# Kernel optimization log

Measured on AMD Instinct MI355X. Metric: run time of the kernel, lower is better.

## Reference

```python
import jax, jax.numpy as jnp
import numpy as np

B, N, DIM = 2, 2048, 1024
NUM_HEADS = 16
EFF = NUM_HEADS // 2          # 8 effective heads
HD = DIM // NUM_HEADS         # 64
LAMBDA_INIT = 0.8
EPS = 1e-5


def setup_inputs() -> dict:
    key = jax.random.key(0)
    ks = jax.random.split(key, 16)
    s = 0.02
    return {
        "x":  jax.random.normal(ks[0], (B, N, DIM), dtype=jnp.float32),
        "Wq": jax.random.normal(ks[1], (DIM, DIM), dtype=jnp.float32) * s,
        "bq": jnp.zeros((DIM,), dtype=jnp.float32),
        "Wk": jax.random.normal(ks[2], (DIM, DIM), dtype=jnp.float32) * s,
        "bk": jnp.zeros((DIM,), dtype=jnp.float32),
        "Wv": jax.random.normal(ks[3], (DIM, DIM), dtype=jnp.float32) * s,
        "bv": jnp.zeros((DIM,), dtype=jnp.float32),
        "Wo": jax.random.normal(ks[4], (DIM, DIM), dtype=jnp.float32) * s,
        "bo": jnp.zeros((DIM,), dtype=jnp.float32),
        "norm_w": jnp.ones((2 * HD,), dtype=jnp.float32),
        "lq1": jax.random.normal(ks[5], (HD,), dtype=jnp.float32) * 0.1,
        "lk1": jax.random.normal(ks[6], (HD,), dtype=jnp.float32) * 0.1,
        "lq2": jax.random.normal(ks[7], (HD,), dtype=jnp.float32) * 0.1,
        "lk2": jax.random.normal(ks[8], (HD,), dtype=jnp.float32) * 0.1,
    }


def reference(x, Wq, bq, Wk, bk, Wv, bv, Wo, bo, norm_w, lq1, lk1, lq2, lk2):
    scale = HD ** -0.5
    # projections (torch Linear: y = x @ W.T + b)
    q = (x @ Wq.T + bq).reshape(B, N, NUM_HEADS, HD).transpose(0, 2, 1, 3) * scale  # [B,2E,N,hd]
    k = (x @ Wk.T + bk).reshape(B, N, NUM_HEADS, HD).transpose(0, 2, 1, 3)          # [B,2E,N,hd]
    v = (x @ Wv.T + bv).reshape(B, N, EFF, 2 * HD).transpose(0, 2, 1, 3)            # [B,E,N,2hd]

    scores = jnp.einsum('bhqd,bhkd->bhqk', q, k)              # [B,2E,N,N]
    probs = jax.nn.softmax(scores, axis=-1)
    probs = probs.reshape(B, EFF, 2, N, N)                    # pair consecutive heads

    lam = jnp.exp(jnp.sum(lq1 * lk1)) - jnp.exp(jnp.sum(lq2 * lk2)) + LAMBDA_INIT
    diff = probs[:, :, 0] - lam * probs[:, :, 1]              # [B,E,N,N]

    out = jnp.einsum('behk,bekd->behd'.replace('e','h').replace('hh','h') if False else 'bhqk,bhkd->bhqd', diff, v)  # [B,E,N,2hd]
    # headwise RMSNorm over last dim (2*hd)
    out = out * jax.lax.rsqrt(jnp.mean(out * out, axis=-1, keepdims=True) + EPS) * norm_w
    out = out * (1.0 - LAMBDA_INIT)

    out = out.transpose(0, 2, 1, 3).reshape(B, N, DIM)
    return out @ Wo.T + bo
```

## Files before the change

### kernel.cpp

```cpp
#include <hip/hip_runtime.h>
#include <hip/hip_bf16.h>

#define B_   2
#define N_   2048
#define DIM_ 1024
#define HD_  64
#define DV_  128

typedef __bf16 bf16;
typedef __bf16 bf16x8 __attribute__((ext_vector_type(8)));
typedef __bf16 bf16x4 __attribute__((ext_vector_type(4)));
typedef float  floatx4 __attribute__((ext_vector_type(4)));
typedef float  floatx16 __attribute__((ext_vector_type(16)));
typedef unsigned int uint;
typedef uint uint2v __attribute__((ext_vector_type(2)));
typedef uint uint4v __attribute__((ext_vector_type(4)));

#if __has_builtin(__builtin_amdgcn_exp2f)
#define EXP2(x) __builtin_amdgcn_exp2f(x)
#else
#define EXP2(x) exp2f(x)
#endif

#define QSCALE 0.1803368801111244f

__device__ __forceinline__ void async16(const void* g, void* l) {
  __builtin_amdgcn_global_load_lds(
      (__attribute__((address_space(1))) void*)g,
      (__attribute__((address_space(3))) void*)l, 16, 0, 0);
}

__device__ __forceinline__ uint packbf(float a, float b) {
  unsigned short ul = __builtin_bit_cast(unsigned short, (bf16)a);
  unsigned short uh = __builtin_bit_cast(unsigned short, (bf16)b);
  return (uint)ul | ((uint)uh << 16);
}

__global__ void convert_kernel(const float* __restrict__ x,
                               const float* __restrict__ wq,
                               const float* __restrict__ wk,
                               const float* __restrict__ wv,
                               const float* __restrict__ wo,
                               bf16* __restrict__ dst) {
  const int NX = B_ * N_ * DIM_;
  const int NW = DIM_ * DIM_;
  int i = (blockIdx.x * 256 + threadIdx.x) * 4;
  const float* src;
  int off;
  if (i < NX) { src = x; off = i; }
  else {
    int j = i - NX;
    int w = j >> 20;
    off = j & (NW - 1);
    src = (w == 0) ? wq : (w == 1) ? wk : (w == 2) ? wv : wo;
  }
  float4 v = *(const float4*)(src + off);
  bf16x4 o = { (bf16)v.x, (bf16)v.y, (bf16)v.z, (bf16)v.w };
  *(bf16x4*)(dst + i) = o;
}

__global__ __launch_bounds__(256) void proj_kernel(
    const bf16* __restrict__ xb, const bf16* __restrict__ wall,
    const float* __restrict__ bq, const float* __restrict__ bk,
    const float* __restrict__ bv,
    bf16* __restrict__ qo, bf16* __restrict__ ko, bf16* __restrict__ vt) {
  __shared__ __align__(16) bf16 SM[2 * 128 * 64];
  bf16* At = SM;
  bf16* Bt = SM + 128 * 64;
  const int tid = threadIdx.x, lane = tid & 63, w = tid >> 6;
  const int tm = blockIdx.x, tn = blockIdx.y, z = blockIdx.z;
  const int quad = lane >> 4, l15 = lane & 15;
  const int wm = (w >> 1) * 64, wn = (w & 1) * 64;
  const bf16* Ab = xb + (long)tm * 128 * DIM_;
  const bf16* Bb = wall + (long)z * (DIM_ * DIM_) + (long)tn * 128 * DIM_;
  floatx4 zero = {0.f, 0.f, 0.f, 0.f};
  floatx4 acc[4][4];
#pragma unroll
  for (int i = 0; i < 4; ++i)
#pragma unroll
    for (int j = 0; j < 4; ++j) acc[i][j] = zero;

  for (int kb = 0; kb < DIM_ / 64; ++kb) {
    for (int idx = tid; idx < 1024; idx += 256) {
      int row = idx >> 3, ch = idx & 7, g = ch ^ (row & 7);
      async16(Ab + row * DIM_ + kb * 64 + g * 8, (char*)At + (idx - lane) * 16);
      async16(Bb + row * DIM_ + kb * 64 + g * 8, (char*)Bt + (idx - lane) * 16);
    }
    __syncthreads();
#pragma unroll
    for (int ks = 0; ks < 2; ++ks) {
      bf16x8 af[4], bfm[4];
#pragma unroll
      for (int mt = 0; mt < 4; ++mt) {
        int r = wm + mt * 16 + l15;
        af[mt] = *(const bf16x8*)&At[r * 64 + ((ks * 4 + quad) ^ (r & 7)) * 8];
      }
#pragma unroll
      for (int nt = 0; nt < 4; ++nt) {
        int r = wn + nt * 16 + l15;
        bfm[nt] = *(const bf16x8*)&Bt[r * 64 + ((ks * 4 + quad) ^ (r & 7)) * 8];
      }
#pragma unroll
      for (int mt = 0; mt < 4; ++mt)
#pragma unroll
        for (int nt = 0; nt < 4; ++nt)
          acc[mt][nt] = __builtin_amdgcn_mfma_f32_16x16x32_bf16(
              af[mt], bfm[nt], acc[mt][nt], 0, 0, 0);
    }
    __syncthreads();
  }

  if (z != 2) {
#pragma unroll
    for (int mt = 0; mt < 4; ++mt)
#pragma unroll
      for (int nt = 0; nt < 4; ++nt)
#pragma unroll
        for (int r = 0; r < 4; ++r) {
          int grow = tm * 128 + wm + mt * 16 + quad * 4 + r;
          int gcol = tn * 128 + wn + nt * 16 + l15;
          float v = acc[mt][nt][r];
          if (z == 0) {
            qo[(long)grow * DIM_ + gcol] = (bf16)((v + bq[gcol]) * QSCALE);
          } else {
            ko[(long)grow * DIM_ + gcol] = (bf16)(v + bk[gcol]);
          }
        }
  } else {
    bf16* Vl = SM;
#pragma unroll
    for (int nt = 0; nt < 4; ++nt) {
      int d = wn + nt * 16 + l15;
      float bvv = bv[tn * 128 + d];
      int m = (d & 7) * 2;
#pragma unroll
      for (int mt = 0; mt < 4; ++mt) {
        bf16x4 v4 = { (bf16)(acc[mt][nt][0] + bvv), (bf16)(acc[mt][nt][1] + bvv),
                      (bf16)(acc[mt][nt][2] + bvv), (bf16)(acc[mt][nt][3] + bvv) };
        int c = (wm >> 2) + mt * 4 + quad;
        *(bf16x4*)&Vl[d * 128 + (c ^ m) * 4] = v4;
      }
    }
    __syncthreads();
    const int bb = tm >> 4, e = tn;
    const long rowbase = ((long)(bb * 8 + e) * 128) * (long)N_ + (tm & 15) * 128;
#pragma unroll
    for (int p = 0; p < 8; ++p) {
      int d = p * 16 + (tid >> 4), j = tid & 15;
      int cs = (2 * j) ^ ((d & 7) * 2);
      bf16x8 val = *(const bf16x8*)&Vl[d * 128 + cs * 4];
      *(bf16x8*)&vt[rowbase + (long)d * N_ + j * 8] = val;
    }
  }
}

__global__ __launch_bounds__(256, 2) void attn_kernel(
    const bf16* __restrict__ qb, const bf16* __restrict__ kbuf,
    const bf16* __restrict__ vt,
    const float* __restrict__ lq1, const float* __restrict__ lk1,
    const float* __restrict__ lq2, const float* __restrict__ lk2,
    const float* __restrict__ norm_w, bf16* __restrict__ ao) {
  __shared__ __align__(16) char smem[65536];

  const int tid = threadIdx.x, lane = tid & 63, w = tid >> 6;
  const int qt = blockIdx.x, e = blockIdx.y, b = blockIdx.z;
  const int hl = w & 1, qh = w >> 1;
  const int h = lane >> 5, l31 = lane & 31;
  const int qbase = qt * 64;

  bf16x8 qf[4];
  {
    const bf16* qrp = qb + (long)(b * N_ + qbase + qh * 32 + l31) * DIM_
                      + e * 128 + hl * 64 + h * 8;
#pragma unroll
    for (int c = 0; c < 4; ++c) qf[c] = *(const bf16x8*)(qrp + c * 16);
  }

  const bf16* kbase = kbuf + (long)b * N_ * DIM_ + e * 128;
  const bf16* vbase = vt + (long)(b * 8 + e) * DV_ * N_;

  floatx16 acc[4];
#pragma unroll
  for (int dt = 0; dt < 4; ++dt) acc[dt] = floatx16{};
  float lp = 0.f;

#define STAGE(ktv, bufv)                                                            \
  {                                                                                 \
    int kt_ = (ktv);                                                                \
    char* kdst = smem + (bufv) * 16384;                                             \
    char* vdst = smem + 32768 + (bufv) * 16384;                                     \
    _Pragma("unroll") for (int t = 0; t < 4; ++t) {                                 \
      int idx = tid + t * 256;                                                      \
      int khl = idx >> 9, row = (idx >> 3) & 63, ch = idx & 7;                      \
      int g = ch ^ (row & 7) ^ ((row >> 3) & 3);                                    \
      async16(kbase + ((long)(kt_ * 64 + row)) * DIM_ + khl * 64 + g * 8,           \
              kdst + (idx - lane) * 16);                                            \
    }                                                                               \
    _Pragma("unroll") for (int t = 0; t < 4; ++t) {                                 \
      int idx = tid + t * 256;                                                      \
      int row = idx >> 3, ch = idx & 7;                                             \
      int g = ch ^ (row & 7) ^ ((row >> 3) & 3);                                    \
      async16(vbase + (long)row * N_ + kt_ * 64 + g * 8,                            \
              vdst + (idx - lane) * 16);                                            \
    }                                                                               \
  }

  STAGE(0, 0);

  for (int kt = 0; kt < N_ / 64; ++kt) {
    const int buf = kt & 1;
    __syncthreads();
    if (kt + 1 < N_ / 64) STAGE(kt + 1, buf ^ 1);

    const bf16* Kh = (const bf16*)(smem + buf * 16384) + hl * 4096;
    const bf16* Vb = (const bf16*)(smem + 32768 + buf * 16384);

    bf16x8 kfrag[2][4], vfrag[4][4];
#pragma unroll
    for (int kt2 = 0; kt2 < 2; ++kt2)
#pragma unroll
      for (int c = 0; c < 4; ++c) {
        int row = kt2 * 32 + l31;
        int sw = (c * 2 + h) ^ (row & 7) ^ ((row >> 3) & 3);
        kfrag[kt2][c] = *(const bf16x8*)&Kh[row * 64 + sw * 8];
      }
#pragma unroll
    for (int dt = 0; dt < 4; ++dt)
#pragma unroll
      for (int kc = 0; kc < 4; ++kc) {
        int row = dt * 32 + l31;
        int sw = (kc * 2 + h) ^ (row & 7) ^ ((row >> 3) & 3);
        vfrag[dt][kc] = *(const bf16x8*)&Vb[row * 64 + sw * 8];
      }

    bf16x8 af[2][2];
#pragma unroll
    for (int kt2 = 0; kt2 < 2; ++kt2) {
      floatx16 sv{};
      __builtin_amdgcn_s_setprio(1);
#pragma unroll
      for (int c = 0; c < 4; ++c)
        sv = __builtin_amdgcn_mfma_f32_32x32x16_bf16(kfrag[kt2][c], qf[c], sv, 0, 0, 0);
      __builtin_amdgcn_s_setprio(0);
      float t[16];
      float s = 0.f;
#pragma unroll
      for (int i = 0; i < 16; ++i) { t[i] = EXP2(sv[i]); s += t[i]; }
      lp += s;
      uint d0 = packbf(t[0], t[1]),   d1 = packbf(t[2], t[3]);
      uint d2 = packbf(t[4], t[5]),   d3 = packbf(t[6], t[7]);
      uint d4 = packbf(t[8], t[9]),   d5 = packbf(t[10], t[11]);
      uint d6 = packbf(t[12], t[13]), d7 = packbf(t[14], t[15]);
      uint4v f0, f1;
#if __has_builtin(__builtin_amdgcn_permlane32_swap)
      uint2v r02 = __builtin_amdgcn_permlane32_swap(d0, d2, false, false);
      uint2v r13 = __builtin_amdgcn_permlane32_swap(d1, d3, false, false);
      f0 = uint4v{r02.x, r13.x, r02.y, r13.y};
      uint2v r46 = __builtin_amdgcn_permlane32_swap(d4, d6, false, false);
      uint2v r57 = __builtin_amdgcn_permlane32_swap(d5, d7, false, false);
      f1 = uint4v{r46.x, r57.x, r46.y, r57.y};
#else
      uint e0 = __shfl_xor((int)d0, 32, 64), e1 = __shfl_xor((int)d1, 32, 64);
      uint e2 = __shfl_xor((int)d2, 32, 64), e3 = __shfl_xor((int)d3, 32, 64);
      uint e4 = __shfl_xor((int)d4, 32, 64), e5 = __shfl_xor((int)d5, 32, 64);
      uint e6 = __shfl_xor((int)d6, 32, 64), e7 = __shfl_xor((int)d7, 32, 64);
      f0 = h ? uint4v{e2, e3, d2, d3} : uint4v{d0, d1, e0, e1};
      f1 = h ? uint4v{e6, e7, d6, d7} : uint4v{d4, d5, e4, e5};
#endif
      af[kt2][0] = __builtin_bit_cast(bf16x8, f0);
      af[kt2][1] = __builtin_bit_cast(bf16x8, f1);
    }
    __builtin_amdgcn_s_setprio(1);
#pragma unroll
    for (int dt = 0; dt < 4; ++dt)
#pragma unroll
      for (int kt2 = 0; kt2 < 2; ++kt2)
#pragma unroll
        for (int u = 0; u < 2; ++u)
          acc[dt] = __builtin_amdgcn_mfma_f32_32x32x16_bf16(
              af[kt2][u], vfrag[dt][kt2 * 2 + u], acc[dt], 0, 0, 0);
    __builtin_amdgcn_s_setprio(0);
  }

  lp += __shfl_xor(lp, 32, 64);

  float* Ob = (float*)smem;
  __syncthreads();

  if (hl == 1) {
#pragma unroll
    for (int r = 0; r < 16; ++r) {
      int qloc = (r & 3) + 8 * (r >> 2) + 4 * h;
      float inv = 1.0f / __shfl(lp, qloc, 64);
      float* row = &Ob[(qh * 32 + qloc) * 128 + l31];
#pragma unroll
      for (int dt = 0; dt < 4; ++dt) row[dt * 32] = acc[dt][r] * inv;
    }
  }
  __syncthreads();
  if (hl == 0) {
    float la = lq1[lane] * lk1[lane];
    float lb = lq2[lane] * lk2[lane];
#pragma unroll
    for (int m = 1; m < 64; m <<= 1) {
      la += __shfl_xor(la, m, 64);
      lb += __shfl_xor(lb, m, 64);
    }
    float lam = __expf(la) - __expf(lb) + 0.8f;
    float nw4[4];
#pragma unroll
    for (int dt = 0; dt < 4; ++dt) nw4[dt] = norm_w[dt * 32 + l31] * 0.2f;
#pragma unroll
    for (int r = 0; r < 16; ++r) {
      int qloc = (r & 3) + 8 * (r >> 2) + 4 * h;
      float inv = 1.0f / __shfl(lp, qloc, 64);
      const float* row = &Ob[(qh * 32 + qloc) * 128 + l31];
      float v[4], ss = 0.f;
#pragma unroll
      for (int dt = 0; dt < 4; ++dt) {
        v[dt] = acc[dt][r] * inv - lam * row[dt * 32];
        ss += v[dt] * v[dt];
      }
#pragma unroll
      for (int msk = 1; msk < 32; msk <<= 1) ss += __shfl_xor(ss, msk, 64);
      float rms = rsqrtf(ss * (1.0f / 128.0f) + 1e-5f);
      int n = qbase + qh * 32 + qloc;
      bf16* dst = ao + (long)(b * N_ + n) * DIM_ + e * DV_ + l31;
#pragma unroll
      for (int dt = 0; dt < 4; ++dt) dst[dt * 32] = (bf16)(v[dt] * rms * nw4[dt]);
    }
  }
}

__global__ __launch_bounds__(512) void out_gemm(
    const bf16* __restrict__ ab, const bf16* __restrict__ wo,
    const float* __restrict__ bo, float* __restrict__ out) {
  __shared__ __align__(16) bf16 At[128 * 64];
  __shared__ __align__(16) bf16 Bt[128 * 64];
  const int tid = threadIdx.x, lane = tid & 63, w = tid >> 6;
  const int tm = blockIdx.x, tn = blockIdx.y;
  const int quad = lane >> 4, l15 = lane & 15;
  const int wm = (w & 3) * 32, wn = (w >> 2) * 64;
  const bf16* Ab = ab + (long)tm * 128 * DIM_;
  const bf16* Bb = wo + (long)tn * 128 * DIM_;
  floatx4 zero = {0.f, 0.f, 0.f, 0.f};
  floatx4 acc[2][4];
#pragma unroll
  for (int i = 0; i < 2; ++i)
#pragma unroll
    for (int j = 0; j < 4; ++j) acc[i][j] = zero;

  for (int kb = 0; kb < DIM_ / 64; ++kb) {
    for (int idx = tid; idx < 1024; idx += 512) {
      int row = idx >> 3, ch = idx & 7, g = ch ^ (row & 7);
      async16(Ab + row * DIM_ + kb * 64 + g * 8, (char*)At + (idx - lane) * 16);
      async16(Bb + row * DIM_ + kb * 64 + g * 8, (char*)Bt + (idx - lane) * 16);
    }
    __syncthreads();
#pragma unroll
    for (int ks = 0; ks < 2; ++ks) {
      bf16x8 af[2], bfm[4];
#pragma unroll
      for (int mt = 0; mt < 2; ++mt) {
        int r = wm + mt * 16 + l15;
        af[mt] = *(const bf16x8*)&At[r * 64 + ((ks * 4 + quad) ^ (r & 7)) * 8];
      }
#pragma unroll
      for (int nt = 0; nt < 4; ++nt) {
        int r = wn + nt * 16 + l15;
        bfm[nt] = *(const bf16x8*)&Bt[r * 64 + ((ks * 4 + quad) ^ (r & 7)) * 8];
      }
#pragma unroll
      for (int mt = 0; mt < 2; ++mt)
#pragma unroll
        for (int nt = 0; nt < 4; ++nt)
          acc[mt][nt] = __builtin_amdgcn_mfma_f32_16x16x32_bf16(
              af[mt], bfm[nt], acc[mt][nt], 0, 0, 0);
    }
    __syncthreads();
  }
#pragma unroll
  for (int mt = 0; mt < 2; ++mt)
#pragma unroll
    for (int nt = 0; nt < 4; ++nt)
#pragma unroll
      for (int r = 0; r < 4; ++r) {
        int grow = tm * 128 + wm + mt * 16 + quad * 4 + r;
        int gcol = tn * 128 + wn + nt * 16 + l15;
        out[(long)grow * DIM_ + gcol] = acc[mt][nt][r] + bo[gcol];
      }
}

extern "C" void kernel_launch(void* const* d_in, const int* in_sizes, int n_in,
                              void* d_out, int out_size, void* d_ws, size_t ws_size,
                              hipStream_t stream) {
  const float* x    = (const float*)d_in[0];
  const float* Wq   = (const float*)d_in[1];
  const float* bq   = (const float*)d_in[2];
  const float* Wk   = (const float*)d_in[3];
  const float* bk   = (const float*)d_in[4];
  const float* Wv   = (const float*)d_in[5];
  const float* bv   = (const float*)d_in[6];
  const float* Wo   = (const float*)d_in[7];
  const float* bo   = (const float*)d_in[8];
  const float* nw   = (const float*)d_in[9];
  const float* lq1  = (const float*)d_in[10];
  const float* lk1  = (const float*)d_in[11];
  const float* lq2  = (const float*)d_in[12];
  const float* lk2  = (const float*)d_in[13];

  char* ws = (char*)d_ws;
  bf16* xb   = (bf16*)(ws + 256);
  bf16* wqb  = xb + 4194304;
  bf16* qb   = wqb + 4 * 1048576;
  bf16* kbuf = qb + 4194304;
  bf16* vtb  = kbuf + 4194304;
  bf16* ab   = vtb + 4194304;

  convert_kernel<<<8192, 256, 0, stream>>>(x, Wq, Wk, Wv, Wo, xb);
  proj_kernel<<<dim3(32, 8, 3), 256, 0, stream>>>(xb, wqb, bq, bk, bv, qb, kbuf, vtb);
  attn_kernel<<<dim3(32, 8, 2), 256, 0, stream>>>(qb, kbuf, vtb, lq1, lk1, lq2, lk2,
                                                  nw, ab);
  out_gemm<<<dim3(32, 8), 512, 0, stream>>>(ab, wqb + 3 * 1048576, bo, (float*)d_out);
}
```

Before: 219.9 us.

## Load attention K/V fragments directly from global memory with larger tiles

```diff
diff --git a/kernel.cpp b/kernel.cpp
--- a/kernel.cpp
+++ b/kernel.cpp
@@ -154,19 +154,20 @@
   }
 }
 
-__global__ __launch_bounds__(256, 2) void attn_kernel(
+__global__ __launch_bounds__(512, 2) void attn_kernel(
     const bf16* __restrict__ qb, const bf16* __restrict__ kbuf,
     const bf16* __restrict__ vt,
     const float* __restrict__ lq1, const float* __restrict__ lk1,
     const float* __restrict__ lq2, const float* __restrict__ lk2,
     const float* __restrict__ norm_w, bf16* __restrict__ ao) {
-  __shared__ __align__(16) char smem[65536];
+  __shared__ __align__(16) float Ob[128 * 128];
 
   const int tid = threadIdx.x, lane = tid & 63, w = tid >> 6;
-  const int qt = blockIdx.x, e = blockIdx.y, b = blockIdx.z;
+  const int swz = (blockIdx.x & 7) * 32 + (blockIdx.x >> 3);
+  const int qt = swz & 15, e = (swz >> 4) & 7, b = swz >> 7;
   const int hl = w & 1, qh = w >> 1;
   const int h = lane >> 5, l31 = lane & 31;
-  const int qbase = qt * 64;
+  const int qbase = qt * 128;
 
   bf16x8 qf[4];
   {
@@ -176,62 +177,29 @@
     for (int c = 0; c < 4; ++c) qf[c] = *(const bf16x8*)(qrp + c * 16);
   }
 
-  const bf16* kbase = kbuf + (long)b * N_ * DIM_ + e * 128;
-  const bf16* vbase = vt + (long)(b * 8 + e) * DV_ * N_;
+  const bf16* krow = kbuf + (long)b * N_ * DIM_ + (long)l31 * DIM_
+                     + e * 128 + hl * 64 + h * 8;
+  const bf16* vrow = vt + (long)(b * 8 + e) * DV_ * N_ + (long)l31 * N_ + h * 8;
 
   floatx16 acc[4];
 #pragma unroll
   for (int dt = 0; dt < 4; ++dt) acc[dt] = floatx16{};
   float lp = 0.f;
 
-#define STAGE(ktv, bufv)                                                            \
-  {                                                                                 \
-    int kt_ = (ktv);                                                                \
-    char* kdst = smem + (bufv) * 16384;                                             \
-    char* vdst = smem + 32768 + (bufv) * 16384;                                     \
-    _Pragma("unroll") for (int t = 0; t < 4; ++t) {                                 \
-      int idx = tid + t * 256;                                                      \
-      int khl = idx >> 9, row = (idx >> 3) & 63, ch = idx & 7;                      \
-      int g = ch ^ (row & 7) ^ ((row >> 3) & 3);                                    \
-      async16(kbase + ((long)(kt_ * 64 + row)) * DIM_ + khl * 64 + g * 8,           \
-              kdst + (idx - lane) * 16);                                            \
-    }                                                                               \
-    _Pragma("unroll") for (int t = 0; t < 4; ++t) {                                 \
-      int idx = tid + t * 256;                                                      \
-      int row = idx >> 3, ch = idx & 7;                                             \
-      int g = ch ^ (row & 7) ^ ((row >> 3) & 3);                                    \
-      async16(vbase + (long)row * N_ + kt_ * 64 + g * 8,                            \
-              vdst + (idx - lane) * 16);                                            \
-    }                                                                               \
-  }
-
-  STAGE(0, 0);
-
   for (int kt = 0; kt < N_ / 64; ++kt) {
-    const int buf = kt & 1;
-    __syncthreads();
-    if (kt + 1 < N_ / 64) STAGE(kt + 1, buf ^ 1);
-
-    const bf16* Kh = (const bf16*)(smem + buf * 16384) + hl * 4096;
-    const bf16* Vb = (const bf16*)(smem + 32768 + buf * 16384);
-
     bf16x8 kfrag[2][4], vfrag[4][4];
+    const bf16* kp = krow + (long)kt * 64 * DIM_;
 #pragma unroll
     for (int kt2 = 0; kt2 < 2; ++kt2)
 #pragma unroll
-      for (int c = 0; c < 4; ++c) {
-        int row = kt2 * 32 + l31;
-        int sw = (c * 2 + h) ^ (row & 7) ^ ((row >> 3) & 3);
-        kfrag[kt2][c] = *(const bf16x8*)&Kh[row * 64 + sw * 8];
-      }
+      for (int c = 0; c < 4; ++c)
+        kfrag[kt2][c] = *(const bf16x8*)(kp + (long)kt2 * 32 * DIM_ + c * 16);
+    const bf16* vp = vrow + kt * 64;
 #pragma unroll
     for (int dt = 0; dt < 4; ++dt)
 #pragma unroll
-      for (int kc = 0; kc < 4; ++kc) {
-        int row = dt * 32 + l31;
-        int sw = (kc * 2 + h) ^ (row & 7) ^ ((row >> 3) & 3);
-        vfrag[dt][kc] = *(const bf16x8*)&Vb[row * 64 + sw * 8];
-      }
+      for (int kc = 0; kc < 4; ++kc)
+        vfrag[dt][kc] = *(const bf16x8*)(vp + (long)dt * 32 * N_ + kc * 16);
 
     bf16x8 af[2][2];
 #pragma unroll
@@ -284,9 +252,6 @@
 
   lp += __shfl_xor(lp, 32, 64);
 
-  float* Ob = (float*)smem;
-  __syncthreads();
-
   if (hl == 1) {
 #pragma unroll
     for (int r = 0; r < 16; ++r) {
@@ -419,7 +384,6 @@
 
   convert_kernel<<<8192, 256, 0, stream>>>(x, Wq, Wk, Wv, Wo, xb);
   proj_kernel<<<dim3(32, 8, 3), 256, 0, stream>>>(xb, wqb, bq, bk, bv, qb, kbuf, vtb);
-  attn_kernel<<<dim3(32, 8, 2), 256, 0, stream>>>(qb, kbuf, vtb, lq1, lk1, lq2, lk2,
-                                                  nw, ab);
+  attn_kernel<<<256, 512, 0, stream>>>(qb, kbuf, vtb, lq1, lk1, lq2, lk2, nw, ab);
   out_gemm<<<dim3(32, 8), 512, 0, stream>>>(ab, wqb + 3 * 1048576, bo, (float*)d_out);
 }
```

New measurement: 327.0 us. 1.49x slower.
